# Kernel tuning notes

Hardware: AMD Instinct MI355X
Metric: run time of the kernel (lower is better)

Reference implementation:

```python
import jax, jax.numpy as jnp
import numpy as np
from jax.ops import segment_sum

N_NODES = 100000
N_EDGES = 1600000
HIDDEN = 64
N_LAYERS = 4
N_CLASSES = 10
N_GRAPHS = 512


def setup_inputs() -> dict:
    key = jax.random.key(0)
    ks = jax.random.split(key, 9)
    x = jax.random.normal(ks[0], (N_NODES, HIDDEN), dtype=jnp.float32)
    edge_index = jax.random.randint(ks[1], (2, N_EDGES), 0, N_NODES, dtype=jnp.int32)
    batch = jnp.sort(jax.random.randint(ks[2], (N_NODES,), 0, N_GRAPHS, dtype=jnp.int32))
    s = 0.05
    W_enc = jax.random.normal(ks[3], (HIDDEN, HIDDEN), dtype=jnp.float32) * s
    b_enc = jax.random.normal(ks[4], (HIDDEN,), dtype=jnp.float32) * s
    W_conv = jax.random.normal(ks[5], (N_LAYERS, HIDDEN, HIDDEN), dtype=jnp.float32) * s
    b_conv = jax.random.normal(ks[6], (N_LAYERS, HIDDEN), dtype=jnp.float32) * s
    W_out = jax.random.normal(ks[7], (HIDDEN, N_CLASSES), dtype=jnp.float32) * s
    b_out = jax.random.normal(ks[8], (N_CLASSES,), dtype=jnp.float32) * s
    return {"x": x, "edge_index": edge_index, "batch": batch,
            "W_enc": W_enc, "b_enc": b_enc, "W_conv": W_conv, "b_conv": b_conv,
            "W_out": W_out, "b_out": b_out, "num_graphs": N_GRAPHS}


def reference(x, edge_index, batch, W_enc, b_enc, W_conv, b_conv, W_out, b_out, num_graphs):
    N = x.shape[0]
    src, dst = edge_index[0], edge_index[1]
    # atom_encoder: Linear
    h = x @ W_enc + b_enc
    # GCN symmetric normalization with self-loops (PyG GCNConv default):
    # deg counts incoming edges (dst) plus the self-loop.
    deg = segment_sum(jnp.ones_like(src, dtype=h.dtype), dst, num_segments=N) + 1.0
    deg_inv_sqrt = jax.lax.rsqrt(deg)
    deg_inv = 1.0 / deg  # self-loop norm = d^-1/2 * d^-1/2
    edge_norm = (deg_inv_sqrt[src] * deg_inv_sqrt[dst])[:, None]  # [E,1]
    for l in range(W_conv.shape[0]):
        hl = h @ W_conv[l]                          # [N,H]
        msg = hl[src] * edge_norm                   # gather + normalize [E,H]
        agg = segment_sum(msg, dst, num_segments=N) # scatter-add
        h = agg + hl * deg_inv[:, None] + b_conv[l] # self-loop + bias
        h = jax.nn.silu(h)                          # dropout p=0 / eval: identity
    # global_add_pool over graph ids
    pooled = segment_sum(h, batch, num_segments=num_graphs)  # [G,H]
    # readout: Linear + ReLU (make_mlp with hidden_layers=1)
    out = jax.nn.relu(pooled @ W_out + b_out)
    return out
```

## Files before the change

### kernel.cpp

```cpp
#include <hip/hip_runtime.h>
#include <math.h>

#define HIDDEN 64
#define N_LAYERS 4
#define N_CLASSES 10
#define N_GRAPHS 512
#define BSH 8
#define NPB 256
#define PART_K 2048
#define IDX_CAP 512

typedef _Float16 __h;
typedef __attribute__((ext_vector_type(4))) _Float16 half4;
typedef __attribute__((ext_vector_type(8))) _Float16 half8;
typedef __attribute__((ext_vector_type(4))) float f32x4;

__global__ __launch_bounds__(256) void k_histA(const int* __restrict__ dst,
                                               int* __restrict__ ghist, int E, int NB) {
    __shared__ int hist[512];
    int t = threadIdx.x;
    hist[t] = 0; hist[t + 256] = 0;
    __syncthreads();
    int base = blockIdx.x * PART_K;
    int kend = min(PART_K, E - base);
    for (int k = t; k < kend; k += 256) atomicAdd(&hist[dst[base + k] >> BSH], 1);
    __syncthreads();
    for (int j = t; j < NB; j += 256) {
        int h = hist[j];
        if (h) atomicAdd(&ghist[j], h);
    }
}

__global__ __launch_bounds__(256) void k_bucketscan(const int* __restrict__ ghist,
                                                    int* __restrict__ bucketbase,
                                                    int* __restrict__ gcur, int NB) {
    __shared__ int s[256];
    int t = threadIdx.x;
    int j0 = 2 * t, j1 = 2 * t + 1;
    int h0 = (j0 < NB) ? ghist[j0] : 0;
    int h1 = (j1 < NB) ? ghist[j1] : 0;
    s[t] = h0 + h1; __syncthreads();
    for (int o = 1; o < 256; o <<= 1) {
        int x = (t >= o) ? s[t - o] : 0;
        __syncthreads();
        s[t] += x;
        __syncthreads();
    }
    int base = (t == 0) ? 0 : s[t - 1];
    if (j0 <= NB) { bucketbase[j0] = base;      gcur[j0] = base; }
    if (j1 <= NB) { bucketbase[j1] = base + h0; gcur[j1] = base + h0; }
}

__global__ __launch_bounds__(256) void k_partition(const int* __restrict__ src,
                                                   const int* __restrict__ dst,
                                                   int* __restrict__ gcur,
                                                   int* __restrict__ packed,
                                                   int E, int NB) {
    __shared__ int hist[512];
    __shared__ int scanE[512];
    __shared__ int cur[512];
    __shared__ int delta[512];
    __shared__ int ps[256];
    __shared__ int stage[PART_K];
    __shared__ unsigned short stgj[PART_K];
    int t = threadIdx.x;
    int base = blockIdx.x * PART_K;
    int kend = min(PART_K, E - base);

    hist[t] = 0; hist[t + 256] = 0;
    __syncthreads();
    for (int k = t; k < kend; k += 256) atomicAdd(&hist[dst[base + k] >> BSH], 1);
    __syncthreads();

    int j0 = 2 * t, j1 = j0 + 1;
    int h0 = hist[j0], h1 = hist[j1];
    ps[t] = h0 + h1; __syncthreads();
    for (int o = 1; o < 256; o <<= 1) {
        int x = (t >= o) ? ps[t - o] : 0;
        __syncthreads();
        ps[t] += x;
        __syncthreads();
    }
    int bexc = (t == 0) ? 0 : ps[t - 1];
    scanE[j0] = bexc;
    scanE[j1] = bexc + h0;
    __syncthreads();

    for (int j = t; j < NB; j += 256) {
        int h = hist[j];
        int g = h ? atomicAdd(&gcur[j], h) : 0;
        delta[j] = g - scanE[j];
        cur[j]   = scanE[j];
    }
    __syncthreads();

    for (int k = t; k < kend; k += 256) {
        int d = dst[base + k], s = src[base + k];
        int j = d >> BSH;
        int pos = atomicAdd(&cur[j], 1);
        stage[pos] = (s << BSH) | (d & (NPB - 1));
        stgj[pos]  = (unsigned short)j;
    }
    __syncthreads();

    for (int i = t; i < kend; i += 256) {
        packed[i + delta[stgj[i]]] = stage[i];
    }
}

__global__ __launch_bounds__(256) void k_fill3(const int* __restrict__ packed,
                                               const int* __restrict__ bucketbase,
                                               int* __restrict__ rowptr,
                                               float* __restrict__ dis,
                                               int* __restrict__ csr_src,
                                               int N, int E) {
    __shared__ int cnt[256];
    __shared__ int rp[256];
    int j = blockIdx.x;
    int t = threadIdx.x;
    int node0 = j << BSH;
    int segb = bucketbase[j];
    int sege = bucketbase[j + 1];

    cnt[t] = 0; __syncthreads();
    for (int i = segb + t; i < sege; i += 256) atomicAdd(&cnt[packed[i] & (NPB - 1)], 1);
    __syncthreads();

    int c = cnt[t];
    rp[t] = c; __syncthreads();
    for (int o = 1; o < 256; o <<= 1) {
        int x = (t >= o) ? rp[t - o] : 0;
        __syncthreads();
        rp[t] += x;
        __syncthreads();
    }
    int node = node0 + t;
    int start = segb + rp[t] - c + node;
    if (node < N) {
        rowptr[node] = start;
        dis[node] = rsqrtf((float)c + 1.0f);
        csr_src[start] = node;
        if (node == N - 1) rowptr[N] = E + N;
    }
    __syncthreads();
    cnt[t] = start + 1;
    __syncthreads();
    for (int i = segb + t; i < sege; i += 256) {
        int v = packed[i];
        int slot = atomicAdd(&cnt[v & (NPB - 1)], 1);
        csr_src[slot] = v >> BSH;
    }
}

__device__ __forceinline__ half4 shfl_xor_h4(half4 v, int m) {
    uint2 u = __builtin_bit_cast(uint2, v);
    u.x = __shfl_xor((int)u.x, m);
    u.y = __shfl_xor((int)u.y, m);
    return __builtin_bit_cast(half4, u);
}

__global__ __launch_bounds__(256) void k_prepW(const float* __restrict__ Wconv,
                                               const float* __restrict__ Wenc,
                                               __h* __restrict__ Wh) {
    int idx = blockIdx.x * 256 + threadIdx.x;
    int l = idx >> 12;
    int kn = idx & 4095;
    int k = kn >> 6, n = kn & 63;
    int nt = n >> 4, nl = n & 15;
    int kt = k >> 5, kr = k & 31;
    int quad = kr >> 3, j = kr & 7;
    int lane = quad * 16 + nl;
    int pos = (((nt * 2 + kt) * 64 + lane) << 3) + j;
    float w = (l < N_LAYERS) ? Wconv[(size_t)l * 4096 + kn] : Wenc[kn];
    Wh[(l << 12) + pos] = (__h)w;
}

__global__ __launch_bounds__(256) void k_layer(const int* __restrict__ csr_src,
                                               const int* __restrict__ rowptr,
                                               const float* __restrict__ dis,
                                               const __h* __restrict__ G,
                                               const __h* __restrict__ Wh,
                                               const float* __restrict__ bias,
                                               const int* __restrict__ batch,
                                               __h* __restrict__ Gho,
                                               float* __restrict__ pooled,
                                               int N, int last) {
    __shared__ __attribute__((aligned(16))) __h At[2][16][72];
    __shared__ int sidx[2][IDX_CAP];
    int tid  = threadIdx.x;
    int wave = tid >> 6;
    int lane = tid & 63;
    int tile = wave >> 1;
    int half = wave & 1;
    int trow0 = blockIdx.x * 32 + tile * 16;
    int grp = lane >> 4;
    int f4  = lane & 15;

    int rpi = trow0 + lane;
    int rpv = rowptr[rpi > N ? N : rpi];
    int beg0 = __shfl(rpv, 0);
    int endL = __shfl(rpv, 16);
    int Lc   = endL - beg0; if (Lc > IDX_CAP) Lc = IDX_CAP;

    int t2 = tid & 127;
    const int* __restrict__ gsrc = csr_src + beg0;
    for (int k = t2; k < Lc; k += 128) sidx[tile][k] = gsrc[k];
    __syncthreads();

    const half4 z = {(__h)0.f, (__h)0.f, (__h)0.f, (__h)0.f};
    const int* sp = sidx[tile];
    #pragma unroll 2
    for (int r = 0; r < 8; ++r) {
        int i = half * 8 + r;
        int beg = __shfl(rpv, i);
        int end = __shfl(rpv, i + 1);
        half4 a = z;
        int e = beg + grp;
        while (e < end) {
            int o = e - beg0;
            int s0 =                  (o      < IDX_CAP) ? sp[o]      : csr_src[e];
            int s1 = (e + 4  < end) ? ((o + 4  < IDX_CAP) ? sp[o + 4]  : csr_src[e + 4])  : -1;
            int s2 = (e + 8  < end) ? ((o + 8  < IDX_CAP) ? sp[o + 8]  : csr_src[e + 8])  : -1;
            int s3 = (e + 12 < end) ? ((o + 12 < IDX_CAP) ? sp[o + 12] : csr_src[e + 12]) : -1;
            int s4 = (e + 16 < end) ? ((o + 16 < IDX_CAP) ? sp[o + 16] : csr_src[e + 16]) : -1;
            int s5 = (e + 20 < end) ? ((o + 20 < IDX_CAP) ? sp[o + 20] : csr_src[e + 20]) : -1;
            int s6 = (e + 24 < end) ? ((o + 24 < IDX_CAP) ? sp[o + 24] : csr_src[e + 24]) : -1;
            int s7 = (e + 28 < end) ? ((o + 28 < IDX_CAP) ? sp[o + 28] : csr_src[e + 28]) : -1;
            half4 r0 = ((const half4*)(G + (size_t)s0 * 64))[f4];
            half4 r1 = (s1 >= 0) ? ((const half4*)(G + (size_t)s1 * 64))[f4] : z;
            half4 r2 = (s2 >= 0) ? ((const half4*)(G + (size_t)s2 * 64))[f4] : z;
            half4 r3 = (s3 >= 0) ? ((const half4*)(G + (size_t)s3 * 64))[f4] : z;
            half4 r4 = (s4 >= 0) ? ((const half4*)(G + (size_t)s4 * 64))[f4] : z;
            half4 r5 = (s5 >= 0) ? ((const half4*)(G + (size_t)s5 * 64))[f4] : z;
            half4 r6 = (s6 >= 0) ? ((const half4*)(G + (size_t)s6 * 64))[f4] : z;
            half4 r7 = (s7 >= 0) ? ((const half4*)(G + (size_t)s7 * 64))[f4] : z;
            a += r0; a += r1; a += r2; a += r3;
            a += r4; a += r5; a += r6; a += r7;
            e += 32;
        }
        a += shfl_xor_h4(a, 16);
        a += shfl_xor_h4(a, 32);
        if (grp == 0) {
            int node = trow0 + i;
            float df = (node < N) ? dis[node] : 0.0f;
            __h dd = (__h)df;
            ((half4*)&At[tile][i][0])[f4] = a * dd;
        }
    }
    __syncthreads();

    int quad = grp, nl = f4;
    half8 bf[4][2];
    #pragma unroll
    for (int nt = 0; nt < 4; ++nt)
        #pragma unroll
        for (int kt = 0; kt < 2; ++kt)
            bf[nt][kt] = *(const half8*)(Wh + (((nt * 2 + kt) * 64 + lane) << 3));

    half8 a0 = *(const half8*)&At[tile][nl][quad * 8];
    half8 a1 = *(const half8*)&At[tile][nl][32 + quad * 8];

    f32x4 acc[4];
    #pragma unroll
    for (int nt = 0; nt < 4; ++nt) {
        acc[nt] = (f32x4){0.f, 0.f, 0.f, 0.f};
        acc[nt] = __builtin_amdgcn_mfma_f32_16x16x32_f16(a0, bf[nt][0], acc[nt], 0, 0, 0);
        acc[nt] = __builtin_amdgcn_mfma_f32_16x16x32_f16(a1, bf[nt][1], acc[nt], 0, 0, 0);
    }

    float b[4];
    #pragma unroll
    for (int nt = 0; nt < 4; ++nt) b[nt] = bias[nt * 16 + nl];

    bool own = ((quad >> 1) == half);

    if (!last) {
        if (own) {
            #pragma unroll
            for (int reg = 0; reg < 4; ++reg) {
                int rr = trow0 + quad * 4 + reg;
                if (rr < N) {
                    float ds_ = dis[rr];
                    #pragma unroll
                    for (int nt = 0; nt < 4; ++nt) {
                        float v = acc[nt][reg] + b[nt];
                        v = v / (1.0f + expf(-v));
                        Gho[(size_t)rr * 64 + nt * 16 + nl] = (__h)(ds_ * v);
                    }
                }
            }
        }
    } else {
        if (own) {
            float run[4] = {0.f, 0.f, 0.f, 0.f};
            int cur = -1;
            #pragma unroll
            for (int reg = 0; reg < 4; ++reg) {
                int rr = trow0 + quad * 4 + reg;
                if (rr < N) {
                    int bi = batch[rr];
                    float vals[4];
                    #pragma unroll
                    for (int nt = 0; nt < 4; ++nt) {
                        float v = acc[nt][reg] + b[nt];
                        vals[nt] = v / (1.0f + expf(-v));
                    }
                    if (bi != cur) {
                        if (cur >= 0) {
                            #pragma unroll
                            for (int nt = 0; nt < 4; ++nt)
                                atomicAdd(&pooled[cur * 64 + nt * 16 + nl], run[nt]);
                        }
                        cur = bi;
                        #pragma unroll
                        for (int nt = 0; nt < 4; ++nt) run[nt] = vals[nt];
                    } else {
                        #pragma unroll
                        for (int nt = 0; nt < 4; ++nt) run[nt] += vals[nt];
                    }
                }
            }
            if (cur >= 0) {
                #pragma unroll
                for (int nt = 0; nt < 4; ++nt)
                    atomicAdd(&pooled[cur * 64 + nt * 16 + nl], run[nt]);
            }
        }
    }
}

__global__ __launch_bounds__(256) void k_gemm_mfma(const float* __restrict__ xf,
                                                   const __h* __restrict__ Wh,
                                                   const float* __restrict__ bias,
                                                   const float* __restrict__ dis,
                                                   __h* __restrict__ Gho,
                                                   int N) {
    int wave = threadIdx.x >> 6;
    int lane = threadIdx.x & 63;
    int row0 = (blockIdx.x * 4 + wave) * 32;
    if (row0 >= N) return;
    int quad = lane >> 4, nl = lane & 15;

    half8 bf[4][2];
    #pragma unroll
    for (int nt = 0; nt < 4; ++nt)
        #pragma unroll
        for (int kt = 0; kt < 2; ++kt)
            bf[nt][kt] = *(const half8*)(Wh + (((nt * 2 + kt) * 64 + lane) << 3));

    f32x4 acc[2][4];
    #pragma unroll
    for (int h = 0; h < 2; ++h) {
        int r = row0 + h * 16 + nl; if (r >= N) r = N - 1;
        const float* ap = xf + (size_t)r * 64 + quad * 8;
        float4 v0 = ((const float4*)ap)[0];
        float4 v1 = ((const float4*)ap)[1];
        float4 v2 = ((const float4*)(ap + 32))[0];
        float4 v3 = ((const float4*)(ap + 32))[1];
        half8 a0 = (half8){(__h)v0.x, (__h)v0.y, (__h)v0.z, (__h)v0.w,
                           (__h)v1.x, (__h)v1.y, (__h)v1.z, (__h)v1.w};
        half8 a1 = (half8){(__h)v2.x, (__h)v2.y, (__h)v2.z, (__h)v2.w,
                           (__h)v3.x, (__h)v3.y, (__h)v3.z, (__h)v3.w};
        #pragma unroll
        for (int nt = 0; nt < 4; ++nt) {
            acc[h][nt] = (f32x4){0.f, 0.f, 0.f, 0.f};
            acc[h][nt] = __builtin_amdgcn_mfma_f32_16x16x32_f16(a0, bf[nt][0], acc[h][nt], 0, 0, 0);
            acc[h][nt] = __builtin_amdgcn_mfma_f32_16x16x32_f16(a1, bf[nt][1], acc[h][nt], 0, 0, 0);
        }
    }

    float b[4];
    #pragma unroll
    for (int nt = 0; nt < 4; ++nt) b[nt] = bias[nt * 16 + nl];

    #pragma unroll
    for (int h = 0; h < 2; ++h) {
        #pragma unroll
        for (int reg = 0; reg < 4; ++reg) {
            int rr = row0 + h * 16 + quad * 4 + reg;
            if (rr < N) {
                float ds = dis[rr];
                #pragma unroll
                for (int nt = 0; nt < 4; ++nt) {
                    float v = acc[h][nt][reg] + b[nt];
                    Gho[(size_t)rr * 64 + nt * 16 + nl] = (__h)(ds * v);
                }
            }
        }
    }
}

__global__ __launch_bounds__(256) void k_readout(const float* __restrict__ pooled,
                                                 const float* __restrict__ Wout,
                                                 const float* __restrict__ bout,
                                                 float* __restrict__ out) {
    int idx = blockIdx.x * 256 + threadIdx.x;
    if (idx >= N_GRAPHS * N_CLASSES) return;
    int g = idx / N_CLASSES, c = idx % N_CLASSES;
    float s = bout[c];
    #pragma unroll
    for (int j = 0; j < 64; ++j) s += pooled[g * 64 + j] * Wout[j * N_CLASSES + c];
    out[idx] = fmaxf(s, 0.0f);
}

extern "C" void kernel_launch(void* const* d_in, const int* in_sizes, int n_in,
                              void* d_out, int out_size, void* d_ws, size_t ws_size,
                              hipStream_t stream) {
    const float* x      = (const float*)d_in[0];
    const int*   ei     = (const int*)d_in[1];
    const int*   batch  = (const int*)d_in[2];
    const float* W_enc  = (const float*)d_in[3];
    const float* b_enc  = (const float*)d_in[4];
    const float* W_conv = (const float*)d_in[5];
    const float* b_conv = (const float*)d_in[6];
    const float* W_out  = (const float*)d_in[7];
    const float* b_out  = (const float*)d_in[8];
    float* out = (float*)d_out;

    const int N = in_sizes[2];
    const int E = in_sizes[1] / 2;
    const int* src = ei;
    const int* dst = ei + E;
    const int NB   = (N + NPB - 1) >> BSH;
    const int NBLK = (E + PART_K - 1) / PART_K;

    char* ws = (char*)d_ws;
    size_t off = 0;
    auto alloc = [&](size_t bytes) -> char* {
        char* p = ws + off;
        off += (bytes + 255) & ~(size_t)255;
        return p;
    };
    int*   ghist      = (int*)alloc((size_t)(NB + 1) * sizeof(int));
    int*   bucketbase = (int*)alloc((size_t)(NB + 1) * sizeof(int));
    int*   gcur       = (int*)alloc((size_t)(NB + 1) * sizeof(int));
    int*   packed     = (int*)alloc((size_t)E * sizeof(int));
    int*   csr_src    = (int*)alloc((size_t)(E + N) * sizeof(int));
    int*   rowptr     = (int*)alloc((size_t)(N + 1) * sizeof(int));
    float* dis        = (float*)alloc((size_t)N * sizeof(float));
    __h*   bufA       = (__h*)alloc((size_t)N * HIDDEN * sizeof(__h));
    __h*   bufB       = (__h*)alloc((size_t)N * HIDDEN * sizeof(__h));
    __h*   Wh         = (__h*)alloc((size_t)(N_LAYERS + 1) * 4096 * sizeof(__h));
    float* pooled     = (float*)alloc((size_t)N_GRAPHS * HIDDEN * sizeof(float));
    (void)ws_size;

    hipMemsetAsync(ghist, 0, (size_t)(NB + 1) * sizeof(int), stream);
    hipMemsetAsync(pooled, 0, (size_t)N_GRAPHS * HIDDEN * sizeof(float), stream);

    k_histA     <<<NBLK, 256, 0, stream>>>(dst, ghist, E, NB);
    k_bucketscan<<<1,    256, 0, stream>>>(ghist, bucketbase, gcur, NB);
    k_partition <<<NBLK, 256, 0, stream>>>(src, dst, gcur, packed, E, NB);
    k_fill3     <<<NB,   256, 0, stream>>>(packed, bucketbase, rowptr, dis, csr_src, N, E);
    k_prepW<<<((N_LAYERS + 1) * 4096) / 256, 256, 0, stream>>>(W_conv, W_enc, Wh);

    int gb32 = (N + 127) / 128;
    k_gemm_mfma<<<gb32, 256, 0, stream>>>(x, Wh + (size_t)N_LAYERS * 4096, b_enc,
                                          dis, bufA, N);

    __h* bufs[2] = {bufA, bufB};
    int glayer = (N + 31) / 32;
    for (int l = 0; l < N_LAYERS; ++l) {
        int last = (l == N_LAYERS - 1);
        k_layer<<<glayer, 256, 0, stream>>>(csr_src, rowptr, dis, bufs[l & 1],
                                            Wh + (size_t)l * 4096,
                                            b_conv + (size_t)l * HIDDEN, batch,
                                            bufs[(l + 1) & 1], pooled, N, last);
    }

    k_readout<<<(N_GRAPHS * N_CLASSES + 255) / 256, 256, 0, stream>>>(pooled, W_out, b_out, out);
}
```

Baseline: 349.1 us.

## Map eight lanes per row with 16-byte gathers, removing cross-lane reduction

Restructures the gather-aggregate phase so each wave handles 8 rows at once, with 8 lanes per row each loading a 16-byte half8 slice of a neighbor's feature row. This replaces the earlier scheme of 16 lanes by 4 edge groups, which processed rows sequentially and needed shuffle reductions. It also adds a fully global fallback path when a tile's edge list exceeds the shared index cap, and uses unsigned byte-offset addressing. The intent is wider loads, no xor-shuffle reductions and no serial row loop. The trade-off is load imbalance across rows that share a wave, and fewer edges in flight per row.

```diff
diff --git a/kernel.cpp b/kernel.cpp
--- a/kernel.cpp
+++ b/kernel.cpp
@@ -150,13 +150,6 @@
         int slot = atomicAdd(&cnt[v & (NPB - 1)], 1);
         csr_src[slot] = v >> BSH;
     }
-}
-
-__device__ __forceinline__ half4 shfl_xor_h4(half4 v, int m) {
-    uint2 u = __builtin_bit_cast(uint2, v);
-    u.x = __shfl_xor((int)u.x, m);
-    u.y = __shfl_xor((int)u.y, m);
-    return __builtin_bit_cast(half4, u);
 }
 
 __global__ __launch_bounds__(256) void k_prepW(const float* __restrict__ Wconv,
@@ -193,63 +186,85 @@
     int tile = wave >> 1;
     int half = wave & 1;
     int trow0 = blockIdx.x * 32 + tile * 16;
-    int grp = lane >> 4;
-    int f4  = lane & 15;
+    int g8  = lane >> 3;
+    int f8  = lane & 7;
+    unsigned f8b = (unsigned)f8 * 16u;
 
     int rpi = trow0 + lane;
     int rpv = rowptr[rpi > N ? N : rpi];
     int beg0 = __shfl(rpv, 0);
     int endL = __shfl(rpv, 16);
-    int Lc   = endL - beg0; if (Lc > IDX_CAP) Lc = IDX_CAP;
-
-    int t2 = tid & 127;
-    const int* __restrict__ gsrc = csr_src + beg0;
-    for (int k = t2; k < Lc; k += 128) sidx[tile][k] = gsrc[k];
-    __syncthreads();
-
-    const half4 z = {(__h)0.f, (__h)0.f, (__h)0.f, (__h)0.f};
-    const int* sp = sidx[tile];
-    #pragma unroll 2
-    for (int r = 0; r < 8; ++r) {
-        int i = half * 8 + r;
-        int beg = __shfl(rpv, i);
-        int end = __shfl(rpv, i + 1);
-        half4 a = z;
-        int e = beg + grp;
-        while (e < end) {
-            int o = e - beg0;
-            int s0 =                  (o      < IDX_CAP) ? sp[o]      : csr_src[e];
-            int s1 = (e + 4  < end) ? ((o + 4  < IDX_CAP) ? sp[o + 4]  : csr_src[e + 4])  : -1;
-            int s2 = (e + 8  < end) ? ((o + 8  < IDX_CAP) ? sp[o + 8]  : csr_src[e + 8])  : -1;
-            int s3 = (e + 12 < end) ? ((o + 12 < IDX_CAP) ? sp[o + 12] : csr_src[e + 12]) : -1;
-            int s4 = (e + 16 < end) ? ((o + 16 < IDX_CAP) ? sp[o + 16] : csr_src[e + 16]) : -1;
-            int s5 = (e + 20 < end) ? ((o + 20 < IDX_CAP) ? sp[o + 20] : csr_src[e + 20]) : -1;
-            int s6 = (e + 24 < end) ? ((o + 24 < IDX_CAP) ? sp[o + 24] : csr_src[e + 24]) : -1;
-            int s7 = (e + 28 < end) ? ((o + 28 < IDX_CAP) ? sp[o + 28] : csr_src[e + 28]) : -1;
-            half4 r0 = ((const half4*)(G + (size_t)s0 * 64))[f4];
-            half4 r1 = (s1 >= 0) ? ((const half4*)(G + (size_t)s1 * 64))[f4] : z;
-            half4 r2 = (s2 >= 0) ? ((const half4*)(G + (size_t)s2 * 64))[f4] : z;
-            half4 r3 = (s3 >= 0) ? ((const half4*)(G + (size_t)s3 * 64))[f4] : z;
-            half4 r4 = (s4 >= 0) ? ((const half4*)(G + (size_t)s4 * 64))[f4] : z;
-            half4 r5 = (s5 >= 0) ? ((const half4*)(G + (size_t)s5 * 64))[f4] : z;
-            half4 r6 = (s6 >= 0) ? ((const half4*)(G + (size_t)s6 * 64))[f4] : z;
-            half4 r7 = (s7 >= 0) ? ((const half4*)(G + (size_t)s7 * 64))[f4] : z;
+    int L    = endL - beg0;
+    bool fits = (L <= IDX_CAP);
+
+    if (fits) {
+        int t2 = tid & 127;
+        const int* __restrict__ gsrc = csr_src + beg0;
+        for (int k = t2; k < L; k += 128) sidx[tile][k] = gsrc[k];
+    }
+    __syncthreads();
+
+    int i   = half * 8 + g8;
+    int beg = __shfl(rpv, i);
+    int end = __shfl(rpv, i + 1);
+    int node = trow0 + i;
+
+    const char* Gb = (const char*)G;
+    const half8 z8 = {(__h)0.f, (__h)0.f, (__h)0.f, (__h)0.f,
+                      (__h)0.f, (__h)0.f, (__h)0.f, (__h)0.f};
+    half8 a = z8;
+#define GLOAD(s) (*(const half8*)(Gb + ((((unsigned)(s)) << 7) + f8b)))
+
+    if (fits) {
+        const int* sp = sidx[tile];
+        int e = beg - beg0, ee = end - beg0;
+        for (; e + 8 <= ee; e += 8) {
+            int s0 = sp[e + 0], s1 = sp[e + 1], s2 = sp[e + 2], s3 = sp[e + 3];
+            int s4 = sp[e + 4], s5 = sp[e + 5], s6 = sp[e + 6], s7 = sp[e + 7];
+            half8 r0 = GLOAD(s0), r1 = GLOAD(s1), r2 = GLOAD(s2), r3 = GLOAD(s3);
+            half8 r4 = GLOAD(s4), r5 = GLOAD(s5), r6 = GLOAD(s6), r7 = GLOAD(s7);
             a += r0; a += r1; a += r2; a += r3;
             a += r4; a += r5; a += r6; a += r7;
-            e += 32;
-        }
-        a += shfl_xor_h4(a, 16);
-        a += shfl_xor_h4(a, 32);
-        if (grp == 0) {
-            int node = trow0 + i;
-            float df = (node < N) ? dis[node] : 0.0f;
-            __h dd = (__h)df;
-            ((half4*)&At[tile][i][0])[f4] = a * dd;
-        }
-    }
-    __syncthreads();
-
-    int quad = grp, nl = f4;
+        }
+        if (e < ee) {
+            #pragma unroll
+            for (int k = 0; k < 8; ++k) {
+                int ek = e + k;
+                int ck = ek < ee ? ek : ee - 1;
+                half8 r = GLOAD(sp[ck]);
+                a += (ek < ee) ? r : z8;
+            }
+        }
+    } else {
+        int e = beg, ee = end;
+        for (; e + 8 <= ee; e += 8) {
+            int s0 = csr_src[e + 0], s1 = csr_src[e + 1], s2 = csr_src[e + 2], s3 = csr_src[e + 3];
+            int s4 = csr_src[e + 4], s5 = csr_src[e + 5], s6 = csr_src[e + 6], s7 = csr_src[e + 7];
+            half8 r0 = GLOAD(s0), r1 = GLOAD(s1), r2 = GLOAD(s2), r3 = GLOAD(s3);
+            half8 r4 = GLOAD(s4), r5 = GLOAD(s5), r6 = GLOAD(s6), r7 = GLOAD(s7);
+            a += r0; a += r1; a += r2; a += r3;
+            a += r4; a += r5; a += r6; a += r7;
+        }
+        if (e < ee) {
+            #pragma unroll
+            for (int k = 0; k < 8; ++k) {
+                int ek = e + k;
+                int ck = ek < ee ? ek : ee - 1;
+                half8 r = GLOAD(csr_src[ck]);
+                a += (ek < ee) ? r : z8;
+            }
+        }
+    }
+#undef GLOAD
+
+    float df = (node < N) ? dis[node] : 0.0f;
+    __h dd = (__h)df;
+    half8 dv = {dd, dd, dd, dd, dd, dd, dd, dd};
+    a = a * dv;
+    *(half8*)&At[tile][i][f8 * 8] = a;
+    __syncthreads();
+
+    int quad = lane >> 4, nl = lane & 15;
     half8 bf[4][2];
     #pragma unroll
     for (int nt = 0; nt < 4; ++nt)
```

Result: faster. 319.0 us (-8.6%).
